# Kernel optimization log

Hardware: AMD Instinct MI355X
Metric: run time of the kernel (lower is better)

## Reference

```python
import jax, jax.numpy as jnp
import numpy as np

B, T = 4, 16000
V = 256      # input_channels (token vocab)
R = 256      # residual_channels
S = 512      # skip_channels
O = 256      # output_channels
L = 16       # layers
DIL = 256    # 2 ** (floor(log2(max_dilation=128)) + 1) -- same for every layer (as in source)


def setup_inputs() -> dict:
    key = jax.random.key(0)
    ks = jax.random.split(key, 12)
    tokens = jax.random.randint(ks[0], (B, T), 0, V)
    embed = jax.random.normal(ks[1], (V, R), jnp.float32) * 0.05
    dilate_w = jax.random.normal(ks[2], (L, 2 * R, R, 2), jnp.float32) * 0.05
    dilate_b = jax.random.normal(ks[3], (L, 2 * R), jnp.float32) * 0.01
    res_w = jax.random.normal(ks[4], (L - 1, R, R), jnp.float32) * 0.05
    res_b = jax.random.normal(ks[5], (L - 1, R), jnp.float32) * 0.01
    skip_w = jax.random.normal(ks[6], (L, S, R), jnp.float32) * 0.05
    skip_b = jax.random.normal(ks[7], (L, S), jnp.float32) * 0.01
    conv_out_w = jax.random.normal(ks[8], (O, S), jnp.float32) * 0.05
    conv_end_w = jax.random.normal(ks[9], (O, O), jnp.float32) * 0.05
    return {
        'tokens': tokens, 'embed': embed,
        'dilate_w': dilate_w, 'dilate_b': dilate_b,
        'res_w': res_w, 'res_b': res_b,
        'skip_w': skip_w, 'skip_b': skip_b,
        'conv_out_w': conv_out_w, 'conv_end_w': conv_end_w,
    }


def _wavenet(tokens, embed, dilate_w, dilate_b, res_w, res_b, skip_w, skip_b,
             conv_out_w, conv_end_w):
    x = embed[tokens]                 # [B,T,R]
    x = jnp.transpose(x, (0, 2, 1))   # [B,R,T]
    skip = None
    for l in range(L):
        # causal dilated conv, kernel=2: y[t] = W0 @ x[t-DIL] + W1 @ x[t] + b
        x_shift = jnp.pad(x, ((0, 0), (0, 0), (DIL, 0)))[:, :, :T]
        in_act = (jnp.einsum('oi,bit->bot', dilate_w[l, :, :, 0], x_shift)
                  + jnp.einsum('oi,bit->bot', dilate_w[l, :, :, 1], x)
                  + dilate_b[l][None, :, None])      # [B,2R,T]
        g = in_act[:, :R, :]                          # source uses SAME slice for tanh & sigmoid
        act = jnp.tanh(g) * jax.nn.sigmoid(g)         # [B,R,T]
        if l < L - 1:
            res = jnp.einsum('oi,bit->bot', res_w[l], act) + res_b[l][None, :, None]
            x = res + x
        s = jnp.einsum('si,bit->bst', skip_w[l], act) + skip_b[l][None, :, None]
        skip = s if skip is None else skip + s
    out = jax.nn.relu(skip)
    out = jnp.einsum('os,bst->bot', conv_out_w, out)
    out = jax.nn.relu(out)
    out = jnp.einsum('po,bot->bpt', conv_end_w, out)
    return jax.nn.softmax(out, axis=1)                # softmax over channel dim


def reference(tokens, embed, dilate_w, dilate_b, res_w, res_b, skip_w, skip_b,
              conv_out_w, conv_end_w):
    return _wavenet(tokens, embed, dilate_w, dilate_b, res_w, res_b,
                    skip_w, skip_b, conv_out_w, conv_end_w)
```

## Files before the change

### kernel.cpp

```cpp
#include <hip/hip_runtime.h>
#include <hip/hip_fp16.h>

#define TLEN 16000

typedef _Float16 h16;
typedef __attribute__((ext_vector_type(8))) _Float16 half8;
typedef __attribute__((ext_vector_type(4))) _Float16 half4;
typedef __attribute__((ext_vector_type(4))) float f32x4;

__device__ __forceinline__ float gated_act(float g) {
  float gc = fmaxf(g, -30.0f);
  float e1 = __expf(-gc);
  float e2 = e1 * e1;
  return (1.0f - e2) / ((1.0f + e2) * (1.0f + e1));
}

__global__ __launch_bounds__(256) void prep_k(
    const float* __restrict__ dw, const float* __restrict__ rw,
    const float* __restrict__ sw, const float* __restrict__ cow,
    const float* __restrict__ cew, const float* __restrict__ sb,
    h16* __restrict__ w2h, h16* __restrict__ resh, h16* __restrict__ skiph,
    h16* __restrict__ couth, h16* __restrict__ cendh, float* __restrict__ sbias)
{
  size_t u = (size_t)blockIdx.x * 256 + threadIdx.x;
  if (u < 2097152) {
    int l = (int)(u >> 17);
    int rem = (int)(u & 131071);
    int o = rem >> 9, k = rem & 511;
    float v = (k < 256) ? dw[(((size_t)l * 512 + o) * 256 + k) * 2]
                        : dw[(((size_t)l * 512 + o) * 256 + (k - 256)) * 2 + 1];
    w2h[u] = (h16)v;
    return;
  }
  u -= 2097152;
  if (u < 983040) { resh[u] = (h16)rw[u]; return; }
  u -= 983040;
  if (u < 2097152) {
    int s = (int)(u >> 12);
    int r = (int)(u & 4095);
    int l = r >> 8, c = r & 255;
    skiph[u] = (h16)sw[((size_t)l * 512 + s) * 256 + c];
    return;
  }
  u -= 2097152;
  if (u < 131072) { couth[u] = (h16)cow[u]; return; }
  u -= 131072;
  if (u < 65536) { cendh[u] = (h16)cew[u]; return; }
  u -= 65536;
  if (u < 512) {
    float s = 0.f;
    for (int l = 0; l < 16; l++) s += sb[(size_t)l * 512 + u];
    sbias[u] = s;
  }
}

__global__ __launch_bounds__(256) void embed_k(
    const int* __restrict__ tok, const float* __restrict__ emb, float* __restrict__ x)
{
  const size_t i = (size_t)blockIdx.x * 256 + threadIdx.x;
  const size_t bt = i >> 6;
  const int c4 = (int)(i & 63) * 4;
  const int tk = tok[bt];
  *(f32x4*)(x + bt * 256 + c4) = *(const f32x4*)(emb + (size_t)tk * 256 + c4);
}

template<int KTOT, int MODE>
__global__ __launch_bounds__(256) void gemm_k(
    const void* __restrict__ Ag, const h16* __restrict__ W,
    const float* __restrict__ bias, void* __restrict__ Og,
    float* __restrict__ xres, int Bc)
{
  __shared__ h16 As[64][40];
  __shared__ h16 Bs[128][40];

  const int tid  = threadIdx.x;
  const int b    = blockIdx.z;
  const int t0   = blockIdx.x * 64;
  const int n0   = blockIdx.y * 128;
  const int lane = tid & 63;
  const int wid  = tid >> 6;
  const int wm   = wid >> 1;
  const int wn   = wid & 1;
  const int r16  = lane & 15;
  const int kg   = lane >> 4;

  f32x4 acc[2][4];
#pragma unroll
  for (int i = 0; i < 2; i++)
#pragma unroll
    for (int j = 0; j < 4; j++) acc[i][j] = (f32x4){0.f, 0.f, 0.f, 0.f};

  const int arow = tid >> 2, asub = tid & 3;
  const int brow = tid >> 1, bsub = tid & 1;
  const int t_a  = t0 + arow;

  for (int k0 = 0; k0 < KTOT; k0 += 32) {
    half8 av;
    if constexpr (MODE == 0) {
      const bool sh = (k0 < 256);
      const int c  = (k0 & 255) + asub * 8;
      const int st = sh ? (t_a - 256) : t_a;
      if (st >= 0) {
        const float* src = (const float*)Ag + ((size_t)b * TLEN + st) * 256 + c;
        f32x4 v0 = *(const f32x4*)(src);
        f32x4 v1 = *(const f32x4*)(src + 4);
#pragma unroll
        for (int j = 0; j < 4; j++) { av[j] = (h16)v0[j]; av[j + 4] = (h16)v1[j]; }
      } else {
#pragma unroll
        for (int j = 0; j < 8; j++) av[j] = (h16)0.f;
      }
    } else if constexpr (MODE == 2) {
      const int l = k0 >> 8, kk = k0 & 255;
      const h16* src = (const h16*)Ag + (((size_t)(l * Bc + b)) * TLEN + t_a) * 256 + kk + asub * 8;
      av = *(const half8*)src;
    } else {
      const int stride = (MODE == 3) ? 512 : 256;
      const h16* src = (const h16*)Ag + ((size_t)b * TLEN + t_a) * stride + k0 + asub * 8;
      av = *(const half8*)src;
    }
    *(half8*)&As[arow][asub * 8] = av;

    {
      const h16* src = W + (size_t)(n0 + brow) * KTOT + k0 + bsub * 16;
      *(half8*)&Bs[brow][bsub * 16]     = *(const half8*)(src);
      *(half8*)&Bs[brow][bsub * 16 + 8] = *(const half8*)(src + 8);
    }
    __syncthreads();

    half8 af[2], bf[4];
#pragma unroll
    for (int mi = 0; mi < 2; mi++) af[mi] = *(const half8*)&As[wm * 32 + mi * 16 + r16][kg * 8];
#pragma unroll
    for (int ni = 0; ni < 4; ni++) bf[ni] = *(const half8*)&Bs[wn * 64 + ni * 16 + r16][kg * 8];
#pragma unroll
    for (int mi = 0; mi < 2; mi++)
#pragma unroll
      for (int ni = 0; ni < 4; ni++)
        acc[mi][ni] = __builtin_amdgcn_mfma_f32_16x16x32_f16(af[mi], bf[ni], acc[mi][ni], 0, 0, 0);
    __syncthreads();
  }

#pragma unroll
  for (int mi = 0; mi < 2; mi++) {
    const int tl = t0 + wm * 32 + mi * 16 + kg * 4;
#pragma unroll
    for (int ni = 0; ni < 4; ni++) {
      const int n = n0 + wn * 64 + ni * 16 + r16;
#pragma unroll
      for (int g = 0; g < 4; g++) {
        float v = acc[mi][ni][g];
        const int t = tl + g;
        if constexpr (MODE == 0) {
          v += bias[n];
          ((h16*)Og)[((size_t)b * TLEN + t) * 256 + n] = (h16)gated_act(v);
        } else if constexpr (MODE == 1) {
          const size_t idx = ((size_t)b * TLEN + t) * 256 + n;
          xres[idx] = xres[idx] + v + bias[n];
        } else if constexpr (MODE == 2) {
          v = fmaxf(v + bias[n], 0.f);
          ((h16*)Og)[((size_t)b * TLEN + t) * 512 + n] = (h16)v;
        } else {
          ((h16*)Og)[((size_t)b * TLEN + t) * 256 + n] = (h16)fmaxf(v, 0.f);
        }
      }
    }
  }
}

__global__ __launch_bounds__(256) void head_k(
    const h16* __restrict__ A, const h16* __restrict__ W, float* __restrict__ out)
{
  __shared__ h16 As[32][40];
  __shared__ h16 Bs[256][40];
  __shared__ float lg[32][257];

  const int tid = threadIdx.x;
  const int b   = blockIdx.z;
  const int t0  = blockIdx.x * 32;
  const int lane = tid & 63, wid = tid >> 6;
  const int r16 = lane & 15, kg = lane >> 4;

  f32x4 acc[2][4];
#pragma unroll
  for (int i = 0; i < 2; i++)
#pragma unroll
    for (int j = 0; j < 4; j++) acc[i][j] = (f32x4){0.f, 0.f, 0.f, 0.f};

  const int arow = tid >> 3, asub = tid & 7;

  for (int k0 = 0; k0 < 256; k0 += 32) {
    {
      const h16* src = A + ((size_t)b * TLEN + t0 + arow) * 256 + k0 + asub * 4;
      *(half4*)&As[arow][asub * 4] = *(const half4*)src;
    }
    {
      const h16* src = W + (size_t)tid * 256 + k0;
#pragma unroll
      for (int q = 0; q < 4; q++) *(half8*)&Bs[tid][q * 8] = *(const half8*)(src + q * 8);
    }
    __syncthreads();
    half8 af[2], bf[4];
#pragma unroll
    for (int mi = 0; mi < 2; mi++) af[mi] = *(const half8*)&As[mi * 16 + r16][kg * 8];
#pragma unroll
    for (int ni = 0; ni < 4; ni++) bf[ni] = *(const half8*)&Bs[wid * 64 + ni * 16 + r16][kg * 8];
#pragma unroll
    for (int mi = 0; mi < 2; mi++)
#pragma unroll
      for (int ni = 0; ni < 4; ni++)
        acc[mi][ni] = __builtin_amdgcn_mfma_f32_16x16x32_f16(af[mi], bf[ni], acc[mi][ni], 0, 0, 0);
    __syncthreads();
  }

#pragma unroll
  for (int mi = 0; mi < 2; mi++) {
    const int rl = mi * 16 + kg * 4;
#pragma unroll
    for (int ni = 0; ni < 4; ni++) {
      const int n = wid * 64 + ni * 16 + r16;
#pragma unroll
      for (int g = 0; g < 4; g++) lg[rl + g][n] = acc[mi][ni][g];
    }
  }
  __syncthreads();

  for (int i = 0; i < 8; i++) {
    const int r = wid * 8 + i;
    float v[4];
#pragma unroll
    for (int j = 0; j < 4; j++) v[j] = lg[r][lane + 64 * j];
    float m = fmaxf(fmaxf(v[0], v[1]), fmaxf(v[2], v[3]));
#pragma unroll
    for (int off = 32; off >= 1; off >>= 1) m = fmaxf(m, __shfl_xor(m, off));
    float s = 0.f;
#pragma unroll
    for (int j = 0; j < 4; j++) { v[j] = __expf(v[j] - m); s += v[j]; }
#pragma unroll
    for (int off = 32; off >= 1; off >>= 1) s += __shfl_xor(s, off);
    const float inv = 1.f / s;
#pragma unroll
    for (int j = 0; j < 4; j++) lg[r][lane + 64 * j] = v[j] * inv;
  }
  __syncthreads();

  const int tl = tid & 31, og = tid >> 5;
  for (int j = 0; j < 32; j++) {
    const int o = og * 32 + j;
    out[((size_t)b * 256 + o) * TLEN + t0 + tl] = lg[tl][o];
  }
}

extern "C" void kernel_launch(void* const* d_in, const int* in_sizes, int n_in,
                              void* d_out, int out_size, void* d_ws, size_t ws_size,
                              hipStream_t stream)
{
  const int*   tokens = (const int*)  d_in[0];
  const float* embedw = (const float*)d_in[1];
  const float* dil_w  = (const float*)d_in[2];
  const float* dil_b  = (const float*)d_in[3];
  const float* resw   = (const float*)d_in[4];
  const float* resb   = (const float*)d_in[5];
  const float* skipw  = (const float*)d_in[6];
  const float* skipb  = (const float*)d_in[7];
  const float* coutw  = (const float*)d_in[8];
  const float* cendw  = (const float*)d_in[9];
  float* out = (float*)d_out;

  char* p = (char*)d_ws;
  auto carve = [&](size_t bytes) { char* r = p; p += (bytes + 255) & ~(size_t)255; return r; };
  h16* w2h     = (h16*)carve((size_t)16 * 256 * 512 * 2);
  h16* reshh   = (h16*)carve((size_t)15 * 256 * 256 * 2);
  h16* skiph   = (h16*)carve((size_t)512 * 4096 * 2);
  h16* couth   = (h16*)carve((size_t)256 * 512 * 2);
  h16* cendh   = (h16*)carve((size_t)256 * 256 * 2);
  float* sbias = (float*)carve(512 * 4);
  const size_t fixed = (size_t)(p - (char*)d_ws);

  const size_t perB = (size_t)TLEN * 256 * 4 + (size_t)16 * TLEN * 256 * 2 + 1024;
  int Bc = 4;
  while (Bc > 1 && fixed + (size_t)Bc * perB > ws_size) Bc >>= 1;

  float* xbuf = (float*)carve((size_t)Bc * TLEN * 256 * 4);
  h16*   act  = (h16*) carve((size_t)16 * Bc * TLEN * 256 * 2);
  h16* sk16 = (h16*)xbuf;
  h16* h116 = (h16*)act;

  prep_k<<<dim3((5374464 + 255) / 256), 256, 0, stream>>>(
      dil_w, resw, skipw, coutw, cendw, skipb, w2h, reshh, skiph, couth, cendh, sbias);

  for (int c0 = 0; c0 < 4; c0 += Bc) {
    const int* tk = tokens + (size_t)c0 * TLEN;
    float* op = out + (size_t)c0 * 256 * TLEN;

    embed_k<<<dim3(Bc * 4000), 256, 0, stream>>>(tk, embedw, xbuf);

    for (int l = 0; l < 16; l++) {
      gemm_k<512, 0><<<dim3(250, 2, Bc), 256, 0, stream>>>(
          xbuf, w2h + (size_t)l * 256 * 512, dil_b + (size_t)l * 512,
          act + (size_t)l * Bc * TLEN * 256, nullptr, Bc);
      if (l < 15)
        gemm_k<256, 1><<<dim3(250, 2, Bc), 256, 0, stream>>>(
            act + (size_t)l * Bc * TLEN * 256, reshh + (size_t)l * 256 * 256,
            resb + (size_t)l * 256, nullptr, xbuf, Bc);
    }

    gemm_k<4096, 2><<<dim3(250, 4, Bc), 256, 0, stream>>>(act, skiph, sbias, sk16, nullptr, Bc);
    gemm_k<512, 3><<<dim3(250, 2, Bc), 256, 0, stream>>>(sk16, couth, nullptr, h116, nullptr, Bc);
    head_k<<<dim3(500, 1, Bc), 256, 0, stream>>>(h116, cendh, op);
  }
}
```

Measured before the change: 2.746 ms.

## Fuse residual and skip GEMMs per layer with fp16 padded input and async LDS loads

The residual and skip projections are merged into one per-layer GEMM with concatenated weights. Skip outputs are accumulated into an fp32 buffer, which removes the large final 4096-K skip GEMM and the storage of all 16 layers' activations. The layer input is kept as a zero-padded fp16 copy so the dilated conv reads fp16 directly with no branch. The GEMM kernel now uses 64x256 tiles, double-buffered global_load_lds staging and LDS-transposed vectorized stores. In exchange it adds fp32 read-modify-write traffic on the skip buffer every layer, plus extra init and convert kernels, and fixes the batch chunk at 2.

```diff
diff --git a/kernel.cpp b/kernel.cpp
--- a/kernel.cpp
+++ b/kernel.cpp
@@ -2,11 +2,18 @@
 #include <hip/hip_fp16.h>
 
 #define TLEN 16000
+#define BC 2
+#define XPROWS 16256
 
 typedef _Float16 h16;
 typedef __attribute__((ext_vector_type(8))) _Float16 half8;
 typedef __attribute__((ext_vector_type(4))) _Float16 half4;
 typedef __attribute__((ext_vector_type(4))) float f32x4;
+
+__device__ __forceinline__ void gload16(const void* g, void* l) {
+  __builtin_amdgcn_global_load_lds((const __attribute__((address_space(1))) void*)g,
+                                   (__attribute__((address_space(3))) void*)l, 16, 0, 0);
+}
 
 __device__ __forceinline__ float gated_act(float g) {
   float gc = fmaxf(g, -30.0f);
@@ -19,8 +26,8 @@
     const float* __restrict__ dw, const float* __restrict__ rw,
     const float* __restrict__ sw, const float* __restrict__ cow,
     const float* __restrict__ cew, const float* __restrict__ sb,
-    h16* __restrict__ w2h, h16* __restrict__ resh, h16* __restrict__ skiph,
-    h16* __restrict__ couth, h16* __restrict__ cendh, float* __restrict__ sbias)
+    h16* __restrict__ w2h, h16* __restrict__ rsw, h16* __restrict__ couth,
+    h16* __restrict__ cendh, float* __restrict__ sbias, h16* __restrict__ x16p)
 {
   size_t u = (size_t)blockIdx.x * 256 + threadIdx.x;
   if (u < 2097152) {
@@ -33,16 +40,17 @@
     return;
   }
   u -= 2097152;
-  if (u < 983040) { resh[u] = (h16)rw[u]; return; }
-  u -= 983040;
-  if (u < 2097152) {
-    int s = (int)(u >> 12);
-    int r = (int)(u & 4095);
-    int l = r >> 8, c = r & 255;
-    skiph[u] = (h16)sw[((size_t)l * 512 + s) * 256 + c];
+  if (u < 3145728) {
+    int l = (int)(u / 196608);
+    int r = (int)(u % 196608);
+    int row = r >> 8, c = r & 255;
+    float v;
+    if (row < 256) v = (l < 15) ? rw[((size_t)l * 256 + row) * 256 + c] : 0.f;
+    else           v = sw[((size_t)l * 512 + (row - 256)) * 256 + c];
+    rsw[u] = (h16)v;
     return;
   }
-  u -= 2097152;
+  u -= 3145728;
   if (u < 131072) { couth[u] = (h16)cow[u]; return; }
   u -= 131072;
   if (u < 65536) { cendh[u] = (h16)cew[u]; return; }
@@ -51,120 +59,177 @@
     float s = 0.f;
     for (int l = 0; l < 16; l++) s += sb[(size_t)l * 512 + u];
     sbias[u] = s;
+    return;
+  }
+  u -= 512;
+  if (u < 131072) {
+    int b = (int)(u >> 16), off = (int)(u & 65535);
+    x16p[(size_t)b * XPROWS * 256 + off] = (h16)0.f;
   }
 }
 
 __global__ __launch_bounds__(256) void embed_k(
-    const int* __restrict__ tok, const float* __restrict__ emb, float* __restrict__ x)
-{
+    const int* __restrict__ tok, const float* __restrict__ emb,
+    float* __restrict__ x, h16* __restrict__ x16p)
+{
+  const int b = blockIdx.y;
   const size_t i = (size_t)blockIdx.x * 256 + threadIdx.x;
-  const size_t bt = i >> 6;
+  const int t = (int)(i >> 6);
   const int c4 = (int)(i & 63) * 4;
-  const int tk = tok[bt];
-  *(f32x4*)(x + bt * 256 + c4) = *(const f32x4*)(emb + (size_t)tk * 256 + c4);
+  const int tk = tok[(size_t)b * TLEN + t];
+  f32x4 v = *(const f32x4*)(emb + (size_t)tk * 256 + c4);
+  *(f32x4*)(x + ((size_t)b * TLEN + t) * 256 + c4) = v;
+  half4 hv;
+#pragma unroll
+  for (int j = 0; j < 4; j++) hv[j] = (h16)v[j];
+  *(half4*)(x16p + (size_t)b * XPROWS * 256 + (size_t)(t + 256) * 256 + c4) = hv;
+}
+
+__global__ __launch_bounds__(256) void skipinit_k(
+    const float* __restrict__ sbias, float* __restrict__ skip)
+{
+  const int b = blockIdx.y;
+  const size_t i = (size_t)blockIdx.x * 256 + threadIdx.x;
+  const int t = (int)(i >> 7);
+  const int s4 = (int)(i & 127) * 4;
+  *(f32x4*)(skip + ((size_t)b * TLEN + t) * 512 + s4) = *(const f32x4*)(sbias + s4);
+}
+
+__global__ __launch_bounds__(256) void cvt_k(
+    const float* __restrict__ skip, h16* __restrict__ sk16)
+{
+  const size_t i = ((size_t)blockIdx.y * 8192000) + ((size_t)blockIdx.x * 256 + threadIdx.x) * 4;
+  f32x4 v = *(const f32x4*)(skip + i);
+  half4 hv;
+#pragma unroll
+  for (int j = 0; j < 4; j++) hv[j] = (h16)fmaxf(v[j], 0.f);
+  *(half4*)(sk16 + i) = hv;
 }
 
 template<int KTOT, int MODE>
-__global__ __launch_bounds__(256) void gemm_k(
-    const void* __restrict__ Ag, const h16* __restrict__ W,
-    const float* __restrict__ bias, void* __restrict__ Og,
-    float* __restrict__ xres, int Bc)
-{
-  __shared__ h16 As[64][40];
-  __shared__ h16 Bs[128][40];
+__global__ __launch_bounds__(256) void gemm3_k(
+    const h16* __restrict__ A, const h16* __restrict__ W,
+    const float* __restrict__ bias, h16* __restrict__ o16,
+    float* __restrict__ of32, float* __restrict__ ofskip, int nskip0)
+{
+  constexpr int NT = KTOT / 32;
+  __shared__ h16 As[2][64 * 32];
+  __shared__ h16 Bs[2][256 * 32];
+  __shared__ h16 tbuf[4][16][72];
 
   const int tid  = threadIdx.x;
-  const int b    = blockIdx.z;
-  const int t0   = blockIdx.x * 64;
-  const int n0   = blockIdx.y * 128;
   const int lane = tid & 63;
-  const int wid  = tid >> 6;
-  const int wm   = wid >> 1;
-  const int wn   = wid & 1;
+  const int w    = tid >> 6;
   const int r16  = lane & 15;
   const int kg   = lane >> 4;
-
-  f32x4 acc[2][4];
-#pragma unroll
-  for (int i = 0; i < 2; i++)
+  const int t0   = blockIdx.x * 64;
+  const int by   = blockIdx.y;
+  const int bz   = blockIdx.z;
+  const int srow  = lane >> 2;
+  const int sunit = (lane & 3) * 8;
+
+  const h16* Ab;
+  if constexpr (MODE == 0)      Ab = A + (size_t)bz * XPROWS * 256;
+  else if constexpr (MODE == 1) Ab = A + (size_t)bz * TLEN * 256;
+  else                          Ab = A + (size_t)bz * TLEN * 512;
+  const int n0w = (MODE == 1) ? by * 256 : 0;
+
+  auto stage = [&](int bi, int kk) {
+    const int k0 = kk * 32;
+    {
+      const h16* src;
+      if constexpr (MODE == 0)
+        src = Ab + (size_t)(t0 + w * 16 + srow + (k0 < 256 ? 0 : 256)) * 256 + (k0 & 255) + sunit;
+      else if constexpr (MODE == 1)
+        src = Ab + (size_t)(t0 + w * 16 + srow) * 256 + k0 + sunit;
+      else
+        src = Ab + (size_t)(t0 + w * 16 + srow) * 512 + k0 + sunit;
+      gload16(src, &As[bi][(w * 16) * 32]);
+    }
+#pragma unroll
+    for (int q = 0; q < 4; q++) {
+      const h16* src = W + (size_t)(n0w + w * 64 + q * 16 + srow) * KTOT + k0 + sunit;
+      gload16(src, &Bs[bi][(w * 64 + q * 16) * 32]);
+    }
+  };
+
+  f32x4 acc[4][4];
+#pragma unroll
+  for (int i = 0; i < 4; i++)
 #pragma unroll
     for (int j = 0; j < 4; j++) acc[i][j] = (f32x4){0.f, 0.f, 0.f, 0.f};
 
-  const int arow = tid >> 2, asub = tid & 3;
-  const int brow = tid >> 1, bsub = tid & 1;
-  const int t_a  = t0 + arow;
-
-  for (int k0 = 0; k0 < KTOT; k0 += 32) {
-    half8 av;
-    if constexpr (MODE == 0) {
-      const bool sh = (k0 < 256);
-      const int c  = (k0 & 255) + asub * 8;
-      const int st = sh ? (t_a - 256) : t_a;
-      if (st >= 0) {
-        const float* src = (const float*)Ag + ((size_t)b * TLEN + st) * 256 + c;
-        f32x4 v0 = *(const f32x4*)(src);
-        f32x4 v1 = *(const f32x4*)(src + 4);
-#pragma unroll
-        for (int j = 0; j < 4; j++) { av[j] = (h16)v0[j]; av[j + 4] = (h16)v1[j]; }
-      } else {
-#pragma unroll
-        for (int j = 0; j < 8; j++) av[j] = (h16)0.f;
-      }
-    } else if constexpr (MODE == 2) {
-      const int l = k0 >> 8, kk = k0 & 255;
-      const h16* src = (const h16*)Ag + (((size_t)(l * Bc + b)) * TLEN + t_a) * 256 + kk + asub * 8;
-      av = *(const half8*)src;
-    } else {
-      const int stride = (MODE == 3) ? 512 : 256;
-      const h16* src = (const h16*)Ag + ((size_t)b * TLEN + t_a) * stride + k0 + asub * 8;
-      av = *(const half8*)src;
-    }
-    *(half8*)&As[arow][asub * 8] = av;
-
-    {
-      const h16* src = W + (size_t)(n0 + brow) * KTOT + k0 + bsub * 16;
-      *(half8*)&Bs[brow][bsub * 16]     = *(const half8*)(src);
-      *(half8*)&Bs[brow][bsub * 16 + 8] = *(const half8*)(src + 8);
-    }
-    __syncthreads();
-
-    half8 af[2], bf[4];
-#pragma unroll
-    for (int mi = 0; mi < 2; mi++) af[mi] = *(const half8*)&As[wm * 32 + mi * 16 + r16][kg * 8];
-#pragma unroll
-    for (int ni = 0; ni < 4; ni++) bf[ni] = *(const half8*)&Bs[wn * 64 + ni * 16 + r16][kg * 8];
-#pragma unroll
-    for (int mi = 0; mi < 2; mi++)
+  stage(0, 0);
+  __syncthreads();
+
+  for (int t = 0; t < NT; t++) {
+    const int cur = t & 1;
+    if (t + 1 < NT) stage(cur ^ 1, t + 1);
+    half8 af[4], bf[4];
+#pragma unroll
+    for (int mi = 0; mi < 4; mi++)
+      af[mi] = *(const half8*)&As[cur][(mi * 16 + r16) * 32 + kg * 8];
+#pragma unroll
+    for (int ni = 0; ni < 4; ni++)
+      bf[ni] = *(const half8*)&Bs[cur][(w * 64 + ni * 16 + r16) * 32 + kg * 8];
+#pragma unroll
+    for (int mi = 0; mi < 4; mi++)
 #pragma unroll
       for (int ni = 0; ni < 4; ni++)
         acc[mi][ni] = __builtin_amdgcn_mfma_f32_16x16x32_f16(af[mi], bf[ni], acc[mi][ni], 0, 0, 0);
     __syncthreads();
   }
 
-#pragma unroll
-  for (int mi = 0; mi < 2; mi++) {
-    const int tl = t0 + wm * 32 + mi * 16 + kg * 4;
+  const int rr = lane >> 2;
+  const int cc = (lane & 3) * 16;
+  const bool is_res = (MODE == 1) && (n0w < nskip0);
+
+  if constexpr (MODE == 1) {
+    if (!is_res) {
+#pragma unroll
+      for (int mi = 0; mi < 4; mi++)
+#pragma unroll
+        for (int ni = 0; ni < 4; ni++) {
+          const int s = n0w + w * 64 + ni * 16 + r16 - nskip0;
+#pragma unroll
+          for (int g = 0; g < 4; g++) {
+            const int t = t0 + mi * 16 + kg * 4 + g;
+            const size_t ix = ((size_t)bz * TLEN + t) * 512 + s;
+            ofskip[ix] += acc[mi][ni][g];
+          }
+        }
+      return;
+    }
+  }
+
+#pragma unroll
+  for (int mi = 0; mi < 4; mi++) {
 #pragma unroll
     for (int ni = 0; ni < 4; ni++) {
-      const int n = n0 + wn * 64 + ni * 16 + r16;
+      const int nl = w * 64 + ni * 16 + r16;
 #pragma unroll
       for (int g = 0; g < 4; g++) {
         float v = acc[mi][ni][g];
-        const int t = tl + g;
+        const int t = t0 + mi * 16 + kg * 4 + g;
         if constexpr (MODE == 0) {
-          v += bias[n];
-          ((h16*)Og)[((size_t)b * TLEN + t) * 256 + n] = (h16)gated_act(v);
+          v = gated_act(v + bias[nl]);
         } else if constexpr (MODE == 1) {
-          const size_t idx = ((size_t)b * TLEN + t) * 256 + n;
-          xres[idx] = xres[idx] + v + bias[n];
-        } else if constexpr (MODE == 2) {
-          v = fmaxf(v + bias[n], 0.f);
-          ((h16*)Og)[((size_t)b * TLEN + t) * 512 + n] = (h16)v;
+          const size_t ix = ((size_t)bz * TLEN + t) * 256 + nl;
+          v = of32[ix] + v + bias[nl];
+          of32[ix] = v;
         } else {
-          ((h16*)Og)[((size_t)b * TLEN + t) * 256 + n] = (h16)fmaxf(v, 0.f);
+          v = fmaxf(v, 0.f);
         }
+        tbuf[w][kg * 4 + g][ni * 16 + r16] = (h16)v;
       }
     }
+    h16* dst;
+    if constexpr (MODE == 1)
+      dst = o16 + (size_t)bz * XPROWS * 256 + (size_t)(256 + t0 + mi * 16 + rr) * 256 + w * 64 + cc;
+    else
+      dst = o16 + ((size_t)bz * TLEN + t0 + mi * 16 + rr) * 256 + w * 64 + cc;
+    *(half8*)dst       = *(const half8*)&tbuf[w][rr][cc];
+    *(half8*)(dst + 8) = *(const half8*)&tbuf[w][rr][cc + 8];
   }
 }
 
@@ -176,10 +241,11 @@
   __shared__ float lg[32][257];
 
   const int tid = threadIdx.x;
-  const int b   = blockIdx.z;
+  const int bz  = blockIdx.z;
   const int t0  = blockIdx.x * 32;
   const int lane = tid & 63, wid = tid >> 6;
   const int r16 = lane & 15, kg = lane >> 4;
+  const h16* Ab = A + (size_t)bz * TLEN * 256;
 
   f32x4 acc[2][4];
 #pragma unroll
@@ -191,7 +257,7 @@
 
   for (int k0 = 0; k0 < 256; k0 += 32) {
     {
-      const h16* src = A + ((size_t)b * TLEN + t0 + arow) * 256 + k0 + asub * 4;
+      const h16* src = Ab + (size_t)(t0 + arow) * 256 + k0 + asub * 4;
       *(half4*)&As[arow][asub * 4] = *(const half4*)src;
     }
     {
@@ -247,7 +313,7 @@
   const int tl = tid & 31, og = tid >> 5;
   for (int j = 0; j < 32; j++) {
     const int o = og * 32 + j;
-    out[((size_t)b * 256 + o) * TLEN + t0 + tl] = lg[tl][o];
+    out[((size_t)bz * 256 + o) * TLEN + t0 + tl] = lg[tl][o];
   }
 }
 
@@ -269,44 +335,44 @@
 
   char* p = (char*)d_ws;
   auto carve = [&](size_t bytes) { char* r = p; p += (bytes + 255) & ~(size_t)255; return r; };
-  h16* w2h     = (h16*)carve((size_t)16 * 256 * 512 * 2);
-  h16* reshh   = (h16*)carve((size_t)15 * 256 * 256 * 2);
-  h16* skiph   = (h16*)carve((size_t)512 * 4096 * 2);
-  h16* couth   = (h16*)carve((size_t)256 * 512 * 2);
-  h16* cendh   = (h16*)carve((size_t)256 * 256 * 2);
-  float* sbias = (float*)carve(512 * 4);
-  const size_t fixed = (size_t)(p - (char*)d_ws);
-
-  const size_t perB = (size_t)TLEN * 256 * 4 + (size_t)16 * TLEN * 256 * 2 + 1024;
-  int Bc = 4;
-  while (Bc > 1 && fixed + (size_t)Bc * perB > ws_size) Bc >>= 1;
-
-  float* xbuf = (float*)carve((size_t)Bc * TLEN * 256 * 4);
-  h16*   act  = (h16*) carve((size_t)16 * Bc * TLEN * 256 * 2);
-  h16* sk16 = (h16*)xbuf;
-  h16* h116 = (h16*)act;
-
-  prep_k<<<dim3((5374464 + 255) / 256), 256, 0, stream>>>(
-      dil_w, resw, skipw, coutw, cendw, skipb, w2h, reshh, skiph, couth, cendh, sbias);
-
-  for (int c0 = 0; c0 < 4; c0 += Bc) {
+  h16* w2h      = (h16*)carve((size_t)16 * 256 * 512 * 2);
+  h16* rsw      = (h16*)carve((size_t)16 * 768 * 256 * 2);
+  h16* couth    = (h16*)carve((size_t)256 * 512 * 2);
+  h16* cendh    = (h16*)carve((size_t)256 * 256 * 2);
+  float* sbias  = (float*)carve(512 * 4);
+  float* xf32   = (float*)carve((size_t)BC * TLEN * 256 * 4);
+  h16*  x16p    = (h16*) carve((size_t)BC * XPROWS * 256 * 2);
+  h16*  act     = (h16*) carve((size_t)BC * TLEN * 256 * 2);
+  float* skipf  = (float*)carve((size_t)BC * TLEN * 512 * 4);
+  h16* sk16 = (h16*)xf32;
+  h16* h116 = act;
+
+  prep_k<<<dim3(21762), 256, 0, stream>>>(
+      dil_w, resw, skipw, coutw, cendw, skipb, w2h, rsw, couth, cendh, sbias, x16p);
+
+  for (int c0 = 0; c0 < 4; c0 += BC) {
     const int* tk = tokens + (size_t)c0 * TLEN;
-    float* op = out + (size_t)c0 * 256 * TLEN;
-
-    embed_k<<<dim3(Bc * 4000), 256, 0, stream>>>(tk, embedw, xbuf);
+
+    embed_k<<<dim3(4000, BC), 256, 0, stream>>>(tk, embedw, xf32, x16p);
+    skipinit_k<<<dim3(8000, BC), 256, 0, stream>>>(sbias, skipf);
 
     for (int l = 0; l < 16; l++) {
-      gemm_k<512, 0><<<dim3(250, 2, Bc), 256, 0, stream>>>(
-          xbuf, w2h + (size_t)l * 256 * 512, dil_b + (size_t)l * 512,
-          act + (size_t)l * Bc * TLEN * 256, nullptr, Bc);
+      gemm3_k<512, 0><<<dim3(250, 1, BC), 256, 0, stream>>>(
+          x16p, w2h + (size_t)l * 131072, dil_b + (size_t)l * 512,
+          act, nullptr, nullptr, 0);
       if (l < 15)
-        gemm_k<256, 1><<<dim3(250, 2, Bc), 256, 0, stream>>>(
-            act + (size_t)l * Bc * TLEN * 256, reshh + (size_t)l * 256 * 256,
-            resb + (size_t)l * 256, nullptr, xbuf, Bc);
-    }
-
-    gemm_k<4096, 2><<<dim3(250, 4, Bc), 256, 0, stream>>>(act, skiph, sbias, sk16, nullptr, Bc);
-    gemm_k<512, 3><<<dim3(250, 2, Bc), 256, 0, stream>>>(sk16, couth, nullptr, h116, nullptr, Bc);
-    head_k<<<dim3(500, 1, Bc), 256, 0, stream>>>(h116, cendh, op);
-  }
-}
+        gemm3_k<256, 1><<<dim3(250, 3, BC), 256, 0, stream>>>(
+            act, rsw + (size_t)l * 196608, resb + (size_t)l * 256,
+            x16p, xf32, skipf, 256);
+      else
+        gemm3_k<256, 1><<<dim3(250, 2, BC), 256, 0, stream>>>(
+            act, rsw + (size_t)15 * 196608 + 65536, nullptr,
+            x16p, xf32, skipf, 0);
+    }
+
+    cvt_k<<<dim3(8000, BC), 256, 0, stream>>>(skipf, sk16);
+    gemm3_k<512, 2><<<dim3(250, 1, BC), 256, 0, stream>>>(
+        sk16, couth, nullptr, h116, nullptr, nullptr, 0);
+    head_k<<<dim3(500, 1, BC), 256, 0, stream>>>(h116, cendh, out + (size_t)c0 * 256 * TLEN);
+  }
+}
```

Result: faster. 2.472 ms (-10.0%).
